# Kernel optimization log

Measured on AMD Instinct MI355X. Metric: run time of the kernel, lower is better.

Reference implementation:

```python
import jax, jax.numpy as jnp
import numpy as np

D_MODEL = 768
D_STATE = 16
D_CONV = 4
EXPAND = 2
D_INNER = EXPAND * D_MODEL          # 1536
DT_RANK = (D_MODEL + 15) // 16      # 48 (mamba default: ceil(d_model/16))


def setup_inputs() -> dict:
    key = jax.random.key(0)
    ks = jax.random.split(key, 8)
    B, T = 2, 1024
    s = 0.02
    return {
        "x": jax.random.normal(ks[0], (B, T, D_MODEL), jnp.float32),
        "ln_g": jnp.ones((D_MODEL,), jnp.float32),
        "ln_b": jnp.zeros((D_MODEL,), jnp.float32),
        "W_in": jax.random.normal(ks[1], (2 * D_INNER, D_MODEL), jnp.float32) * s,
        "conv_w": jax.random.normal(ks[2], (D_INNER, 1, D_CONV), jnp.float32) * s,
        "conv_b": jnp.zeros((D_INNER,), jnp.float32),
        "W_xproj": jax.random.normal(ks[3], (DT_RANK + 2 * D_STATE, D_INNER), jnp.float32) * s,
        "W_dt": jax.random.normal(ks[4], (D_INNER, DT_RANK), jnp.float32) * s,
        "b_dt": jax.random.normal(ks[5], (D_INNER,), jnp.float32) * s,
        "A_log": jnp.log(jnp.broadcast_to(jnp.arange(1.0, D_STATE + 1.0, dtype=jnp.float32), (D_INNER, D_STATE))),
        "Dp": jnp.ones((D_INNER,), jnp.float32),
        "W_out": jax.random.normal(ks[6], (D_MODEL, D_INNER), jnp.float32) * s,
    }


def _mamba_block(x, ln_g, ln_b, W_in, conv_w, conv_b, W_xproj, W_dt, b_dt, A_log, Dp, W_out):
    B, T, D = x.shape
    # LayerNorm
    mu = x.mean(-1, keepdims=True)
    var = ((x - mu) ** 2).mean(-1, keepdims=True)
    h = (x - mu) * jax.lax.rsqrt(var + 1e-5) * ln_g + ln_b
    # in_proj -> [B,T,2*d_inner], split into x-branch and gate z
    xz = h @ W_in.T
    xs, z = jnp.split(xz, 2, axis=-1)
    # causal depthwise conv over time (pad left d_conv-1), then SiLU
    xc = jax.lax.conv_general_dilated(
        xs.transpose(0, 2, 1), conv_w, (1,), [(D_CONV - 1, 0)],
        dimension_numbers=("NCH", "OIH", "NCH"), feature_group_count=D_INNER)
    xc = jax.nn.silu(xc.transpose(0, 2, 1) + conv_b)  # [B,T,d_inner]
    # x_proj -> dt_rank + 2*d_state
    x_dbl = xc @ W_xproj.T
    dt_r = x_dbl[..., :DT_RANK]
    Bm = x_dbl[..., DT_RANK:DT_RANK + D_STATE]       # [B,T,n]
    Cm = x_dbl[..., DT_RANK + D_STATE:]              # [B,T,n]
    dt = jax.nn.softplus(dt_r @ W_dt.T + b_dt)       # [B,T,d_inner]
    A = -jnp.exp(A_log)                              # [d_inner, n]
    dA = jnp.exp(jnp.einsum("btd,dn->btdn", dt, A))  # [B,T,d,n]
    dBu = jnp.einsum("btd,btn->btdn", dt * xc, Bm)   # [B,T,d,n]

    def step(s, inp):
        dA_t, dBu_t, C_t = inp
        s = dA_t * s + dBu_t                          # [B,d,n]
        y_t = jnp.einsum("bdn,bn->bd", s, C_t)
        return s, y_t

    s0 = jnp.zeros((B, D_INNER, D_STATE), x.dtype)
    _, ys = jax.lax.scan(step, s0,
                         (dA.transpose(1, 0, 2, 3), dBu.transpose(1, 0, 2, 3), Cm.transpose(1, 0, 2)))
    y = ys.transpose(1, 0, 2) + Dp * xc              # D skip connection
    y = y * jax.nn.silu(z)                           # gate
    return x + y @ W_out.T                           # out_proj + residual


def reference(x, ln_g, ln_b, W_in, conv_w, conv_b, W_xproj, W_dt, b_dt, A_log, Dp, W_out):
    return _mamba_block(x, ln_g, ln_b, W_in, conv_w, conv_b, W_xproj, W_dt, b_dt, A_log, Dp, W_out)
```

## Files before the change

kernel.cpp:

```cpp
#include <hip/hip_runtime.h>

typedef unsigned short u16;
typedef unsigned int u32;
typedef __attribute__((ext_vector_type(8))) short short8;
typedef __attribute__((ext_vector_type(4))) float f32x4;

#define D_MODEL 768
#define D_INNER 1536
#define D_XZ    3072
#define D_STATE 16
#define DT_RANK 48
#define NROW    2048
#define SEQ     1024
#define XDS     128
#define NCHUNK  128
#define CLEN    8

typedef const __attribute__((address_space(1))) u32 glb_u32;
typedef __attribute__((address_space(3))) u32 lds_u32;

__device__ __forceinline__ float bf2f(u16 u) {
    union { unsigned int i; float f; } v; v.i = ((unsigned int)u) << 16; return v.f;
}
__device__ __forceinline__ u16 f2bf(float f) {
    union { float f; unsigned int i; } v; v.f = f;
    unsigned int r = v.i + 0x7fffu + ((v.i >> 16) & 1u);
    return (u16)(r >> 16);
}
__device__ __forceinline__ void g2lds16(const u16* g, u16* l) {
    __builtin_amdgcn_global_load_lds((glb_u32*)g, (lds_u32*)l, 16, 0, 0);
}

#define N0 (D_XZ * D_MODEL / 4)
#define N1 (D_MODEL * D_INNER / 4)
#define N2 (XDS * D_INNER / 4)
#define N3 (D_INNER * 64 / 4)
#define N4 (D_INNER * D_STATE / 4)
#define N5 (NROW * XDS / 4)
#define N6 (NROW * D_MODEL / 4)
#define PREP_BLOCKS ((N0+N1+N2+N3+N4+N5+N6) / 256)
__global__ __launch_bounds__(256) void prep_ln_k(
    const float* __restrict__ x, const float* __restrict__ g,
    const float* __restrict__ bln, u16* __restrict__ h,
    const float* __restrict__ W_in, const float* __restrict__ W_out,
    const float* __restrict__ W_xp, const float* __restrict__ W_dt,
    const float* __restrict__ A_log,
    u16* __restrict__ Win_bf, u16* __restrict__ Wout_bf,
    u16* __restrict__ Wxp_bf, u16* __restrict__ Wdt_bf,
    float* __restrict__ negA, float* __restrict__ xdbl,
    float* __restrict__ outz)
{
    __shared__ float sred[4], sqred[4];
    int tid = threadIdx.x;
    if (blockIdx.x < NROW) {
        int row = blockIdx.x;
        const float* xr = x + (size_t)row * D_MODEL;
        float v[3], s = 0.f, sq = 0.f;
#pragma unroll
        for (int j = 0; j < 3; ++j) {
            v[j] = xr[tid + j * 256];
            s += v[j]; sq += v[j] * v[j];
        }
#pragma unroll
        for (int off = 32; off >= 1; off >>= 1) {
            s  += __shfl_xor(s,  off, 64);
            sq += __shfl_xor(sq, off, 64);
        }
        if ((tid & 63) == 0) { sred[tid >> 6] = s; sqred[tid >> 6] = sq; }
        __syncthreads();
        float st = sred[0] + sred[1] + sred[2] + sred[3];
        float sqt = sqred[0] + sqred[1] + sqred[2] + sqred[3];
        float mu = st * (1.f / D_MODEL);
        float var = sqt * (1.f / D_MODEL) - mu * mu;
        float rstd = rsqrtf(var + 1e-5f);
        u16* hr = h + (size_t)row * D_MODEL;
#pragma unroll
        for (int j = 0; j < 3; ++j) {
            int idx = tid + j * 256;
            hr[idx] = f2bf((v[j] - mu) * rstd * g[idx] + bln[idx]);
        }
        return;
    }
    int gid = (blockIdx.x - NROW) * 256 + tid;
    if (gid < N0) {
        float4 v = *(const float4*)(W_in + (size_t)gid * 4);
        u16* o = Win_bf + (size_t)gid * 4;
        o[0]=f2bf(v.x); o[1]=f2bf(v.y); o[2]=f2bf(v.z); o[3]=f2bf(v.w);
    } else if (gid < N0 + N1) {
        int i = gid - N0;
        float4 v = *(const float4*)(W_out + (size_t)i * 4);
        u16* o = Wout_bf + (size_t)i * 4;
        o[0]=f2bf(v.x); o[1]=f2bf(v.y); o[2]=f2bf(v.z); o[3]=f2bf(v.w);
    } else if (gid < N0 + N1 + N2) {
        int i = gid - N0 - N1;
        int n = (i * 4) / D_INNER, k = (i * 4) % D_INNER;
        u16* o = Wxp_bf + (size_t)i * 4;
        if (n < 80) {
            float4 v = *(const float4*)(W_xp + (size_t)n * D_INNER + k);
            o[0]=f2bf(v.x); o[1]=f2bf(v.y); o[2]=f2bf(v.z); o[3]=f2bf(v.w);
        } else { o[0]=0; o[1]=0; o[2]=0; o[3]=0; }
    } else if (gid < N0 + N1 + N2 + N3) {
        int i = gid - N0 - N1 - N2;
        int r = (i * 4) >> 6, c0 = (i * 4) & 63;
        u16* o = Wdt_bf + (size_t)i * 4;
        if (c0 < DT_RANK) {
            float4 v = *(const float4*)(W_dt + (size_t)r * DT_RANK + c0);
            o[0]=f2bf(v.x); o[1]=f2bf(v.y); o[2]=f2bf(v.z); o[3]=f2bf(v.w);
        } else { o[0]=0; o[1]=0; o[2]=0; o[3]=0; }
    } else if (gid < N0 + N1 + N2 + N3 + N4) {
        int i = gid - N0 - N1 - N2 - N3;
        float4 v = *(const float4*)(A_log + (size_t)i * 4);
        *(float4*)(negA + (size_t)i * 4) =
            make_float4(-__expf(v.x), -__expf(v.y), -__expf(v.z), -__expf(v.w));
    } else if (gid < N0 + N1 + N2 + N3 + N4 + N5) {
        int i = gid - N0 - N1 - N2 - N3 - N4;
        *(float4*)(xdbl + (size_t)i * 4) = make_float4(0.f, 0.f, 0.f, 0.f);
    } else {
        int i = gid - N0 - N1 - N2 - N3 - N4 - N5;
        *(float4*)(outz + (size_t)i * 4) = make_float4(0.f, 0.f, 0.f, 0.f);
    }
}

template<int MT, int NT, bool OUT_BF16>
__global__ __launch_bounds__(256) void gemm128(
    const u16* __restrict__ A, const u16* __restrict__ B,
    void* __restrict__ Cv, int M, int N, int K)
{
    constexpr int BM = 32 * MT, BN = 32 * NT;
    __shared__ __align__(16) u16 As[BM * 32];
    __shared__ __align__(16) u16 Bs[BN * 32];
    int tid = threadIdx.x, w = tid >> 6, lane = tid & 63;
    int wm = w & 1, wn = w >> 1;
    int m0 = blockIdx.x * BM, n0 = blockIdx.y * BN;
    int mloc = lane & 15, quad = lane >> 4;
    int lr = lane >> 2, lc = lane & 3;
    f32x4 acc[MT][NT] = {};

    for (int k0 = 0; k0 < K; k0 += 32) {
        __syncthreads();
#pragma unroll
        for (int j = w; j < 2 * MT; j += 4) {
            int row = j * 16 + lr;
            int cb = lc ^ ((row >> 1) & 3);
            g2lds16(A + (size_t)(m0 + row) * K + k0 + cb * 8, &As[j * 512]);
        }
#pragma unroll
        for (int j = w; j < 2 * NT; j += 4) {
            int row = j * 16 + lr;
            int cb = lc ^ ((row >> 1) & 3);
            g2lds16(B + (size_t)(n0 + row) * K + k0 + cb * 8, &Bs[j * 512]);
        }
        __syncthreads();
        short8 afr[MT], bfr[NT];
#pragma unroll
        for (int mt = 0; mt < MT; ++mt) {
            int row = wm * MT * 16 + mt * 16 + mloc;
            int cb = quad ^ ((row >> 1) & 3);
            afr[mt] = *(const short8*)(&As[row * 32 + cb * 8]);
        }
#pragma unroll
        for (int nt = 0; nt < NT; ++nt) {
            int row = wn * NT * 16 + nt * 16 + mloc;
            int cb = quad ^ ((row >> 1) & 3);
            bfr[nt] = *(const short8*)(&Bs[row * 32 + cb * 8]);
        }
#pragma unroll
        for (int mt = 0; mt < MT; ++mt)
#pragma unroll
            for (int nt = 0; nt < NT; ++nt)
                acc[mt][nt] = __builtin_amdgcn_mfma_f32_16x16x32_bf16(
                    afr[mt], bfr[nt], acc[mt][nt], 0, 0, 0);
    }
#pragma unroll
    for (int mt = 0; mt < MT; ++mt) {
        int grow0 = m0 + wm * MT * 16 + mt * 16 + quad * 4;
#pragma unroll
        for (int nt = 0; nt < NT; ++nt) {
            int gcol = n0 + wn * NT * 16 + nt * 16 + mloc;
#pragma unroll
            for (int r = 0; r < 4; ++r) {
                size_t idx = (size_t)(grow0 + r) * N + gcol;
                float v = acc[mt][nt][r];
                if (OUT_BF16) ((u16*)Cv)[idx] = f2bf(v);
                else          ((float*)Cv)[idx] = v;
            }
        }
    }
}

template<int MT, int NT, int KSLICE, bool ADD_X>
__global__ __launch_bounds__(256) void gemm_splitk(
    const u16* __restrict__ A, const u16* __restrict__ B,
    const float* __restrict__ X, float* __restrict__ Cout, int K, int CS)
{
    constexpr int BM = 32 * MT, BN = 32 * NT;
    __shared__ __align__(16) u16 As[BM * 32];
    __shared__ __align__(16) u16 Bs[BN * 32];
    int tid = threadIdx.x, w = tid >> 6, lane = tid & 63;
    int wm = w & 1, wn = w >> 1;
    int m0 = blockIdx.x * BM, n0 = blockIdx.y * BN;
    int kbase = blockIdx.z * KSLICE;
    int mloc = lane & 15, quad = lane >> 4;
    int lr = lane >> 2, lc = lane & 3;
    f32x4 acc[MT][NT] = {};

    for (int k0 = 0; k0 < KSLICE; k0 += 32) {
        __syncthreads();
#pragma unroll
        for (int j = w; j < 2 * MT; j += 4) {
            int row = j * 16 + lr;
            int cb = lc ^ ((row >> 1) & 3);
            g2lds16(A + (size_t)(m0 + row) * K + kbase + k0 + cb * 8, &As[j * 512]);
        }
#pragma unroll
        for (int j = w; j < 2 * NT; j += 4) {
            int row = j * 16 + lr;
            int cb = lc ^ ((row >> 1) & 3);
            g2lds16(B + (size_t)(n0 + row) * K + kbase + k0 + cb * 8, &Bs[j * 512]);
        }
        __syncthreads();
        short8 afr[MT], bfr[NT];
#pragma unroll
        for (int mt = 0; mt < MT; ++mt) {
            int row = wm * MT * 16 + mt * 16 + mloc;
            int cb = quad ^ ((row >> 1) & 3);
            afr[mt] = *(const short8*)(&As[row * 32 + cb * 8]);
        }
#pragma unroll
        for (int nt = 0; nt < NT; ++nt) {
            int row = wn * NT * 16 + nt * 16 + mloc;
            int cb = quad ^ ((row >> 1) & 3);
            bfr[nt] = *(const short8*)(&Bs[row * 32 + cb * 8]);
        }
#pragma unroll
        for (int mt = 0; mt < MT; ++mt)
#pragma unroll
            for (int nt = 0; nt < NT; ++nt)
                acc[mt][nt] = __builtin_amdgcn_mfma_f32_16x16x32_bf16(
                    afr[mt], bfr[nt], acc[mt][nt], 0, 0, 0);
    }
#pragma unroll
    for (int mt = 0; mt < MT; ++mt) {
        int grow0 = m0 + wm * MT * 16 + mt * 16 + quad * 4;
#pragma unroll
        for (int nt = 0; nt < NT; ++nt) {
            int gcol = n0 + wn * NT * 16 + nt * 16 + mloc;
#pragma unroll
            for (int r = 0; r < 4; ++r) {
                size_t idx = (size_t)(grow0 + r) * CS + gcol;
                float v = acc[mt][nt][r];
                if (ADD_X && blockIdx.z == 0) v += X[idx];
                unsafeAtomicAdd(&Cout[idx], v);
            }
        }
    }
}

__global__ __launch_bounds__(256) void dtgemm_k(
    const float* __restrict__ xdbl, const u16* __restrict__ Wdt,
    const float* __restrict__ bias, u16* __restrict__ dtout)
{
    __shared__ __align__(16) u16 Bs[64 * 72];
    int tid = threadIdx.x, wave = tid >> 6, lane = tid & 63;
    int m0 = blockIdx.x * 64, n0 = blockIdx.y * 64;
    int mloc = lane & 15, quad = lane >> 4;
    {
        int r = tid >> 3, ck = (tid & 7) * 8;
#pragma unroll
        for (int rr = 0; rr < 64; rr += 32) {
            int4 bv = *(const int4*)(Wdt + (size_t)(n0 + r + rr) * 64 + ck);
            *(int4*)(&Bs[(r + rr) * 72 + ck]) = bv;
        }
    }
    int arow = m0 + wave * 16 + mloc;
    const float* ar = xdbl + (size_t)arow * XDS + quad * 8;
    short8 af[2];
#pragma unroll
    for (int h = 0; h < 2; ++h) {
        float4 a0 = *(const float4*)(ar + h * 32);
        float4 a1 = *(const float4*)(ar + h * 32 + 4);
        short8 t;
        t[0]=(short)f2bf(a0.x); t[1]=(short)f2bf(a0.y);
        t[2]=(short)f2bf(a0.z); t[3]=(short)f2bf(a0.w);
        t[4]=(short)f2bf(a1.x); t[5]=(short)f2bf(a1.y);
        t[6]=(short)f2bf(a1.z); t[7]=(short)f2bf(a1.w);
        af[h] = t;
    }
    __syncthreads();
    f32x4 acc[4] = {};
#pragma unroll
    for (int h = 0; h < 2; ++h)
#pragma unroll
        for (int nt = 0; nt < 4; ++nt) {
            short8 bf = *(const short8*)(&Bs[(nt * 16 + mloc) * 72 + h * 32 + quad * 8]);
            acc[nt] = __builtin_amdgcn_mfma_f32_16x16x32_bf16(af[h], bf, acc[nt], 0, 0, 0);
        }
#pragma unroll
    for (int nt = 0; nt < 4; ++nt) {
        int gcol = n0 + nt * 16 + mloc;
        int grow = m0 + wave * 16 + quad * 4;
#pragma unroll
        for (int r = 0; r < 4; ++r) {
            float t = acc[nt][r] + bias[gcol];
            float sp = (t > 15.f) ? t : __logf(1.f + __expf(t));
            dtout[(size_t)(grow + r) * D_INNER + gcol] = f2bf(sp);
        }
    }
}

__global__ __launch_bounds__(256) void conv_silu_k(
    const u16* __restrict__ xz, const float* __restrict__ cw,
    const float* __restrict__ cb, u16* __restrict__ xc)
{
    int gid = blockIdx.x * 256 + threadIdx.x;
    int r = gid / (D_INNER / 4);
    int c4 = (gid - r * (D_INNER / 4)) * 4;
    int t = r & (SEQ - 1);
    float4 cbv = *(const float4*)(cb + c4);
    float acc[4] = {cbv.x, cbv.y, cbv.z, cbv.w};
    float4 wv[4];
#pragma unroll
    for (int j = 0; j < 4; ++j) wv[j] = *(const float4*)(cw + (c4 + j) * 4);
#pragma unroll
    for (int k = 0; k < 4; ++k) {
        int tt = t - 3 + k;
        if (tt >= 0) {
            ushort4 xv = *(const ushort4*)(xz + (size_t)(r - 3 + k) * D_XZ + c4);
            acc[0] += bf2f(xv.x) * ((const float*)&wv[0])[k];
            acc[1] += bf2f(xv.y) * ((const float*)&wv[1])[k];
            acc[2] += bf2f(xv.z) * ((const float*)&wv[2])[k];
            acc[3] += bf2f(xv.w) * ((const float*)&wv[3])[k];
        }
    }
    ushort4 o;
    o.x = f2bf(acc[0] / (1.f + __expf(-acc[0])));
    o.y = f2bf(acc[1] / (1.f + __expf(-acc[1])));
    o.z = f2bf(acc[2] / (1.f + __expf(-acc[2])));
    o.w = f2bf(acc[3] / (1.f + __expf(-acc[3])));
    *(ushort4*)(xc + (size_t)r * D_INNER + c4) = o;
}

__global__ __launch_bounds__(256) void scan_p1(
    const u16* __restrict__ dt, const u16* __restrict__ xc,
    const float* __restrict__ xdbl, const float* __restrict__ negA,
    float* __restrict__ Sbuf, float* __restrict__ dtsumbuf)
{
    __shared__ float Bsh[CLEN][D_STATE];
    int tid = threadIdx.x;
    int gid = blockIdx.x * 256 + tid;
    int d = gid % D_INNER;
    int bcN = gid / D_INNER;
    int c = bcN % NCHUNK, b = bcN / NCHUNK;
    size_t r0 = (size_t)b * SEQ + c * CLEN;
    if (tid < CLEN * D_STATE) {
        int tt = tid >> 4, n = tid & 15;
        Bsh[tt][n] = xdbl[(r0 + tt) * XDS + DT_RANK + n];
    }
    float a[D_STATE], s[D_STATE] = {};
    {
        const float4* Ar = (const float4*)(negA + d * D_STATE);
        float4 a0 = Ar[0], a1 = Ar[1], a2 = Ar[2], a3 = Ar[3];
        a[0]=a0.x; a[1]=a0.y; a[2]=a0.z; a[3]=a0.w;
        a[4]=a1.x; a[5]=a1.y; a[6]=a1.z; a[7]=a1.w;
        a[8]=a2.x; a[9]=a2.y; a[10]=a2.z; a[11]=a2.w;
        a[12]=a3.x; a[13]=a3.y; a[14]=a3.z; a[15]=a3.w;
    }
    float dtv[CLEN], du[CLEN];
    const u16* dp = dt + r0 * D_INNER + d;
    const u16* xp = xc + r0 * D_INNER + d;
#pragma unroll
    for (int t = 0; t < CLEN; ++t) {
        dtv[t] = bf2f(dp[t * D_INNER]);
        du[t] = dtv[t] * bf2f(xp[t * D_INNER]);
    }
    __syncthreads();
    float dtsum = 0.f;
#pragma unroll
    for (int t = 0; t < CLEN; ++t) {
        dtsum += dtv[t];
#pragma unroll
        for (int n = 0; n < D_STATE; ++n)
            s[n] = __expf(dtv[t] * a[n]) * s[n] + du[t] * Bsh[t][n];
    }
    float4* So = (float4*)(Sbuf + (size_t)gid * D_STATE);
#pragma unroll
    for (int j = 0; j < 4; ++j)
        So[j] = make_float4(s[j*4], s[j*4+1], s[j*4+2], s[j*4+3]);
    dtsumbuf[gid] = dtsum;
}

__global__ __launch_bounds__(256) void scan_p2(
    const float* __restrict__ Sbuf, const float* __restrict__ dtsumbuf,
    const float* __restrict__ negA, float* __restrict__ carry)
{
    int gid = blockIdx.x * 256 + threadIdx.x;
    int n = gid % D_STATE;
    int d = (gid / D_STATE) % D_INNER;
    int b = gid / (D_STATE * D_INNER);
    float a = negA[d * D_STATE + n];
    float s = 0.f;
#pragma unroll 8
    for (int c = 0; c < NCHUNK; ++c) {
        size_t idx = ((size_t)(b * NCHUNK + c) * D_INNER + d);
        carry[idx * D_STATE + n] = s;
        s = Sbuf[idx * D_STATE + n] + __expf(a * dtsumbuf[idx]) * s;
    }
}

__global__ __launch_bounds__(256) void scan_p3(
    const u16* __restrict__ dt, const u16* __restrict__ xc,
    const u16* __restrict__ xz, const float* __restrict__ xdbl,
    const float* __restrict__ negA, const float* __restrict__ Dp,
    const float* __restrict__ carry, u16* __restrict__ yy)
{
    __shared__ float BCsh[CLEN][2 * D_STATE];
    int tid = threadIdx.x;
    int gid = blockIdx.x * 256 + tid;
    int d = gid % D_INNER;
    int bcN = gid / D_INNER;
    int c = bcN % NCHUNK, b = bcN / NCHUNK;
    size_t r0 = (size_t)b * SEQ + c * CLEN;
    {
        int tt = tid >> 5, j = tid & 31;
        BCsh[tt][j] = xdbl[(r0 + tt) * XDS + DT_RANK + j];
    }
    float a[D_STATE], s[D_STATE];
    {
        const float4* Ci = (const float4*)(carry + (size_t)gid * D_STATE);
        float4 c0 = Ci[0], c1 = Ci[1], c2 = Ci[2], c3 = Ci[3];
        s[0]=c0.x; s[1]=c0.y; s[2]=c0.z; s[3]=c0.w;
        s[4]=c1.x; s[5]=c1.y; s[6]=c1.z; s[7]=c1.w;
        s[8]=c2.x; s[9]=c2.y; s[10]=c2.z; s[11]=c2.w;
        s[12]=c3.x; s[13]=c3.y; s[14]=c3.z; s[15]=c3.w;
        const float4* Ar = (const float4*)(negA + d * D_STATE);
        float4 a0 = Ar[0], a1 = Ar[1], a2 = Ar[2], a3 = Ar[3];
        a[0]=a0.x; a[1]=a0.y; a[2]=a0.z; a[3]=a0.w;
        a[4]=a1.x; a[5]=a1.y; a[6]=a1.z; a[7]=a1.w;
        a[8]=a2.x; a[9]=a2.y; a[10]=a2.z; a[11]=a2.w;
        a[12]=a3.x; a[13]=a3.y; a[14]=a3.z; a[15]=a3.w;
    }
    float dtv[CLEN], xcv[CLEN], zv[CLEN];
    const u16* dp = dt + r0 * D_INNER + d;
    const u16* xp = xc + r0 * D_INNER + d;
    const u16* zp = xz + r0 * D_XZ + D_INNER + d;
#pragma unroll
    for (int t = 0; t < CLEN; ++t) {
        dtv[t] = bf2f(dp[t * D_INNER]);
        xcv[t] = bf2f(xp[t * D_INNER]);
        zv[t]  = bf2f(zp[t * D_XZ]);
    }
    float dpv = Dp[d];
    __syncthreads();
    u16* yp = yy + r0 * D_INNER + d;
#pragma unroll
    for (int t = 0; t < CLEN; ++t) {
        float du = dtv[t] * xcv[t];
        float y = 0.f;
#pragma unroll
        for (int n = 0; n < D_STATE; ++n) {
            s[n] = __expf(dtv[t] * a[n]) * s[n] + du * BCsh[t][n];
            y += s[n] * BCsh[t][D_STATE + n];
        }
        float yv = y + dpv * xcv[t];
        float sig = 1.f / (1.f + __expf(-zv[t]));
        yp[t * D_INNER] = f2bf(yv * (zv[t] * sig));
    }
}

extern "C" void kernel_launch(void* const* d_in, const int* in_sizes, int n_in,
                              void* d_out, int out_size, void* d_ws, size_t ws_size,
                              hipStream_t stream) {
    const float* x      = (const float*)d_in[0];
    const float* ln_g   = (const float*)d_in[1];
    const float* ln_b   = (const float*)d_in[2];
    const float* W_in   = (const float*)d_in[3];
    const float* conv_w = (const float*)d_in[4];
    const float* conv_b = (const float*)d_in[5];
    const float* W_xp   = (const float*)d_in[6];
    const float* W_dt   = (const float*)d_in[7];
    const float* b_dt   = (const float*)d_in[8];
    const float* A_log  = (const float*)d_in[9];
    const float* Dp     = (const float*)d_in[10];
    const float* W_out  = (const float*)d_in[11];
    float* out = (float*)d_out;

    char* ws = (char*)d_ws;
    u16*   h_bf    = (u16*)ws;   ws += (size_t)NROW * D_MODEL * 2;
    u16*   xz_bf   = (u16*)ws;   ws += (size_t)NROW * D_XZ * 2;
    u16*   xc_bf   = (u16*)ws;   ws += (size_t)NROW * D_INNER * 2;
    float* xdbl    = (float*)ws; ws += (size_t)NROW * XDS * 4;
    u16*   dtbuf   = (u16*)ws;   ws += (size_t)NROW * D_INNER * 2;
    u16*   yybuf   = (u16*)ws;   ws += (size_t)NROW * D_INNER * 2;
    u16*   Win_bf  = (u16*)ws;   ws += (size_t)D_XZ * D_MODEL * 2;
    u16*   Wout_bf = (u16*)ws;   ws += (size_t)D_MODEL * D_INNER * 2;
    u16*   Wxp_bf  = (u16*)ws;   ws += (size_t)XDS * D_INNER * 2;
    u16*   Wdt_bf  = (u16*)ws;   ws += (size_t)D_INNER * 64 * 2;
    float* negA    = (float*)ws; ws += (size_t)D_INNER * D_STATE * 4;
    float* Sbuf    = (float*)ws; ws += (size_t)2 * NCHUNK * D_INNER * 16 * 4;
    float* dtsumb  = (float*)ws; ws += (size_t)2 * NCHUNK * D_INNER * 4;
    float* carryb  = (float*)ws;

    prep_ln_k<<<NROW + PREP_BLOCKS, 256, 0, stream>>>(
        x, ln_g, ln_b, h_bf, W_in, W_out, W_xp, W_dt, A_log,
        Win_bf, Wout_bf, Wxp_bf, Wdt_bf, negA, xdbl, out);

    gemm128<4, 2, true><<<dim3(NROW / 128, D_XZ / 64), 256, 0, stream>>>(
        h_bf, Win_bf, xz_bf, NROW, D_XZ, D_MODEL);
    conv_silu_k<<<NROW * (D_INNER / 4) / 256, 256, 0, stream>>>(
        xz_bf, conv_w, conv_b, xc_bf);
    gemm_splitk<2, 4, 192, false><<<dim3(NROW / 64, 1, 8), 256, 0, stream>>>(
        xc_bf, Wxp_bf, nullptr, xdbl, D_INNER, XDS);
    dtgemm_k<<<dim3(NROW / 64, D_INNER / 64), 256, 0, stream>>>(
        xdbl, Wdt_bf, b_dt, dtbuf);

    scan_p1<<<2 * NCHUNK * D_INNER / 256, 256, 0, stream>>>(
        dtbuf, xc_bf, xdbl, negA, Sbuf, dtsumb);
    scan_p2<<<2 * D_INNER * D_STATE / 256, 256, 0, stream>>>(
        Sbuf, dtsumb, negA, carryb);
    scan_p3<<<2 * NCHUNK * D_INNER / 256, 256, 0, stream>>>(
        dtbuf, xc_bf, xz_bf, xdbl, negA, Dp, carryb, yybuf);

    gemm_splitk<2, 2, 768, true><<<dim3(NROW / 64, D_MODEL / 64, 2), 256, 0, stream>>>(
        yybuf, Wout_bf, x, out, D_INNER, D_MODEL);
}
```

Baseline: 206.6 us.

## Fuse three-phase chunked scan into one cooperative kernel with grid syncs

Merges the chunk-local scan, the cross-chunk carry propagation and the output pass into a single cooperative kernel separated by grid-wide syncs. It keeps dt, xc, z and B/C in registers and LDS across phases instead of reloading them. Chunk length doubles and the chunk count halves so that 768 blocks can be co-resident, with launch bounds set to 3 blocks per CU. The costs are grid-sync overhead, higher register pressure from holding 16-step arrays, and a serial carry phase that only 192 of the 768 blocks execute.

```diff
diff --git a/kernel.cpp b/kernel.cpp
--- a/kernel.cpp
+++ b/kernel.cpp
@@ -1,4 +1,7 @@
 #include <hip/hip_runtime.h>
+#include <hip/hip_cooperative_groups.h>
+
+namespace cg = cooperative_groups;
 
 typedef unsigned short u16;
 typedef unsigned int u32;
@@ -13,8 +16,8 @@
 #define NROW    2048
 #define SEQ     1024
 #define XDS     128
-#define NCHUNK  128
-#define CLEN    8
+#define NCHUNK  64
+#define CLEN    16
 
 typedef const __attribute__((address_space(1))) u32 glb_u32;
 typedef __attribute__((address_space(3))) u32 lds_u32;
@@ -340,23 +343,28 @@
     *(ushort4*)(xc + (size_t)r * D_INNER + c4) = o;
 }
 
-__global__ __launch_bounds__(256) void scan_p1(
+__global__ __launch_bounds__(256, 3) void scan_fused(
     const u16* __restrict__ dt, const u16* __restrict__ xc,
-    const float* __restrict__ xdbl, const float* __restrict__ negA,
-    float* __restrict__ Sbuf, float* __restrict__ dtsumbuf)
+    const u16* __restrict__ xz, const float* __restrict__ xdbl,
+    const float* __restrict__ negA, const float* __restrict__ Dp,
+    float* __restrict__ Sbuf, float* __restrict__ dtsumbuf,
+    float* __restrict__ carry, u16* __restrict__ yy)
 {
-    __shared__ float Bsh[CLEN][D_STATE];
+    __shared__ float BCsh[CLEN][2 * D_STATE];
+    cg::grid_group grid = cg::this_grid();
     int tid = threadIdx.x;
     int gid = blockIdx.x * 256 + tid;
     int d = gid % D_INNER;
     int bcN = gid / D_INNER;
     int c = bcN % NCHUNK, b = bcN / NCHUNK;
     size_t r0 = (size_t)b * SEQ + c * CLEN;
-    if (tid < CLEN * D_STATE) {
-        int tt = tid >> 4, n = tid & 15;
-        Bsh[tt][n] = xdbl[(r0 + tt) * XDS + DT_RANK + n];
-    }
-    float a[D_STATE], s[D_STATE] = {};
+#pragma unroll
+    for (int j = 0; j < 2; ++j) {
+        int idx = tid + j * 256;
+        int row = idx >> 5, col = idx & 31;
+        BCsh[row][col] = xdbl[(r0 + row) * XDS + DT_RANK + col];
+    }
+    float a[D_STATE];
     {
         const float4* Ar = (const float4*)(negA + d * D_STATE);
         float4 a0 = Ar[0], a1 = Ar[1], a2 = Ar[2], a3 = Ar[3];
@@ -365,105 +373,75 @@
         a[8]=a2.x; a[9]=a2.y; a[10]=a2.z; a[11]=a2.w;
         a[12]=a3.x; a[13]=a3.y; a[14]=a3.z; a[15]=a3.w;
     }
-    float dtv[CLEN], du[CLEN];
-    const u16* dp = dt + r0 * D_INNER + d;
-    const u16* xp = xc + r0 * D_INNER + d;
-#pragma unroll
-    for (int t = 0; t < CLEN; ++t) {
-        dtv[t] = bf2f(dp[t * D_INNER]);
-        du[t] = dtv[t] * bf2f(xp[t * D_INNER]);
-    }
+    float dtv[CLEN], xcv[CLEN], zv[CLEN];
+    {
+        const u16* dp = dt + r0 * D_INNER + d;
+        const u16* xp = xc + r0 * D_INNER + d;
+        const u16* zp = xz + r0 * D_XZ + D_INNER + d;
+#pragma unroll
+        for (int t = 0; t < CLEN; ++t) {
+            dtv[t] = bf2f(dp[t * D_INNER]);
+            xcv[t] = bf2f(xp[t * D_INNER]);
+            zv[t]  = bf2f(zp[t * D_XZ]);
+        }
+    }
+    float dpv = Dp[d];
     __syncthreads();
-    float dtsum = 0.f;
-#pragma unroll
-    for (int t = 0; t < CLEN; ++t) {
-        dtsum += dtv[t];
-#pragma unroll
-        for (int n = 0; n < D_STATE; ++n)
-            s[n] = __expf(dtv[t] * a[n]) * s[n] + du[t] * Bsh[t][n];
-    }
-    float4* So = (float4*)(Sbuf + (size_t)gid * D_STATE);
-#pragma unroll
-    for (int j = 0; j < 4; ++j)
-        So[j] = make_float4(s[j*4], s[j*4+1], s[j*4+2], s[j*4+3]);
-    dtsumbuf[gid] = dtsum;
-}
-
-__global__ __launch_bounds__(256) void scan_p2(
-    const float* __restrict__ Sbuf, const float* __restrict__ dtsumbuf,
-    const float* __restrict__ negA, float* __restrict__ carry)
-{
-    int gid = blockIdx.x * 256 + threadIdx.x;
-    int n = gid % D_STATE;
-    int d = (gid / D_STATE) % D_INNER;
-    int b = gid / (D_STATE * D_INNER);
-    float a = negA[d * D_STATE + n];
-    float s = 0.f;
+    {
+        float s[D_STATE] = {};
+        float dtsum = 0.f;
+#pragma unroll
+        for (int t = 0; t < CLEN; ++t) {
+            dtsum += dtv[t];
+            float du = dtv[t] * xcv[t];
+#pragma unroll
+            for (int n = 0; n < D_STATE; ++n)
+                s[n] = __expf(dtv[t] * a[n]) * s[n] + du * BCsh[t][n];
+        }
+        float4* So = (float4*)(Sbuf + (size_t)gid * D_STATE);
+#pragma unroll
+        for (int j = 0; j < 4; ++j)
+            So[j] = make_float4(s[j*4], s[j*4+1], s[j*4+2], s[j*4+3]);
+        dtsumbuf[gid] = dtsum;
+    }
+    grid.sync();
+    if (blockIdx.x < (2 * D_INNER * D_STATE) / 256) {
+        int g2 = blockIdx.x * 256 + tid;
+        int n2 = g2 % D_STATE;
+        int d2 = (g2 / D_STATE) % D_INNER;
+        int b2 = g2 / (D_STATE * D_INNER);
+        float a2 = negA[d2 * D_STATE + n2];
+        float s = 0.f;
 #pragma unroll 8
-    for (int c = 0; c < NCHUNK; ++c) {
-        size_t idx = ((size_t)(b * NCHUNK + c) * D_INNER + d);
-        carry[idx * D_STATE + n] = s;
-        s = Sbuf[idx * D_STATE + n] + __expf(a * dtsumbuf[idx]) * s;
-    }
-}
-
-__global__ __launch_bounds__(256) void scan_p3(
-    const u16* __restrict__ dt, const u16* __restrict__ xc,
-    const u16* __restrict__ xz, const float* __restrict__ xdbl,
-    const float* __restrict__ negA, const float* __restrict__ Dp,
-    const float* __restrict__ carry, u16* __restrict__ yy)
-{
-    __shared__ float BCsh[CLEN][2 * D_STATE];
-    int tid = threadIdx.x;
-    int gid = blockIdx.x * 256 + tid;
-    int d = gid % D_INNER;
-    int bcN = gid / D_INNER;
-    int c = bcN % NCHUNK, b = bcN / NCHUNK;
-    size_t r0 = (size_t)b * SEQ + c * CLEN;
+        for (int cc = 0; cc < NCHUNK; ++cc) {
+            size_t idx = ((size_t)(b2 * NCHUNK + cc) * D_INNER + d2);
+            carry[idx * D_STATE + n2] = s;
+            s = Sbuf[idx * D_STATE + n2] + __expf(a2 * dtsumbuf[idx]) * s;
+        }
+    }
+    grid.sync();
     {
-        int tt = tid >> 5, j = tid & 31;
-        BCsh[tt][j] = xdbl[(r0 + tt) * XDS + DT_RANK + j];
-    }
-    float a[D_STATE], s[D_STATE];
-    {
+        float s[D_STATE];
         const float4* Ci = (const float4*)(carry + (size_t)gid * D_STATE);
         float4 c0 = Ci[0], c1 = Ci[1], c2 = Ci[2], c3 = Ci[3];
         s[0]=c0.x; s[1]=c0.y; s[2]=c0.z; s[3]=c0.w;
         s[4]=c1.x; s[5]=c1.y; s[6]=c1.z; s[7]=c1.w;
         s[8]=c2.x; s[9]=c2.y; s[10]=c2.z; s[11]=c2.w;
         s[12]=c3.x; s[13]=c3.y; s[14]=c3.z; s[15]=c3.w;
-        const float4* Ar = (const float4*)(negA + d * D_STATE);
-        float4 a0 = Ar[0], a1 = Ar[1], a2 = Ar[2], a3 = Ar[3];
-        a[0]=a0.x; a[1]=a0.y; a[2]=a0.z; a[3]=a0.w;
-        a[4]=a1.x; a[5]=a1.y; a[6]=a1.z; a[7]=a1.w;
-        a[8]=a2.x; a[9]=a2.y; a[10]=a2.z; a[11]=a2.w;
-        a[12]=a3.x; a[13]=a3.y; a[14]=a3.z; a[15]=a3.w;
-    }
-    float dtv[CLEN], xcv[CLEN], zv[CLEN];
-    const u16* dp = dt + r0 * D_INNER + d;
-    const u16* xp = xc + r0 * D_INNER + d;
-    const u16* zp = xz + r0 * D_XZ + D_INNER + d;
-#pragma unroll
-    for (int t = 0; t < CLEN; ++t) {
-        dtv[t] = bf2f(dp[t * D_INNER]);
-        xcv[t] = bf2f(xp[t * D_INNER]);
-        zv[t]  = bf2f(zp[t * D_XZ]);
-    }
-    float dpv = Dp[d];
-    __syncthreads();
-    u16* yp = yy + r0 * D_INNER + d;
-#pragma unroll
-    for (int t = 0; t < CLEN; ++t) {
-        float du = dtv[t] * xcv[t];
-        float y = 0.f;
-#pragma unroll
-        for (int n = 0; n < D_STATE; ++n) {
-            s[n] = __expf(dtv[t] * a[n]) * s[n] + du * BCsh[t][n];
-            y += s[n] * BCsh[t][D_STATE + n];
-        }
-        float yv = y + dpv * xcv[t];
-        float sig = 1.f / (1.f + __expf(-zv[t]));
-        yp[t * D_INNER] = f2bf(yv * (zv[t] * sig));
+        u16* yp = yy + r0 * D_INNER + d;
+#pragma unroll
+        for (int t = 0; t < CLEN; ++t) {
+            float du = dtv[t] * xcv[t];
+            float y = 0.f;
+#pragma unroll
+            for (int n = 0; n < D_STATE; ++n) {
+                s[n] = __expf(dtv[t] * a[n]) * s[n] + du * BCsh[t][n];
+                y += s[n] * BCsh[t][D_STATE + n];
+            }
+            float yv = y + dpv * xcv[t];
+            float sig = 1.f / (1.f + __expf(-zv[t]));
+            yp[t * D_INNER] = f2bf(yv * (zv[t] * sig));
+        }
     }
 }
 
@@ -513,12 +491,16 @@
     dtgemm_k<<<dim3(NROW / 64, D_INNER / 64), 256, 0, stream>>>(
         xdbl, Wdt_bf, b_dt, dtbuf);
 
-    scan_p1<<<2 * NCHUNK * D_INNER / 256, 256, 0, stream>>>(
-        dtbuf, xc_bf, xdbl, negA, Sbuf, dtsumb);
-    scan_p2<<<2 * D_INNER * D_STATE / 256, 256, 0, stream>>>(
-        Sbuf, dtsumb, negA, carryb);
-    scan_p3<<<2 * NCHUNK * D_INNER / 256, 256, 0, stream>>>(
-        dtbuf, xc_bf, xz_bf, xdbl, negA, Dp, carryb, yybuf);
+    {
+        void* args[] = {
+            (void*)&dtbuf, (void*)&xc_bf, (void*)&xz_bf, (void*)&xdbl,
+            (void*)&negA, (void*)&Dp, (void*)&Sbuf, (void*)&dtsumb,
+            (void*)&carryb, (void*)&yybuf
+        };
+        hipLaunchCooperativeKernel((void*)scan_fused,
+                                   dim3(2 * NCHUNK * D_INNER / 256), dim3(256),
+                                   args, 0, stream);
+    }
 
     gemm_splitk<2, 2, 768, true><<<dim3(NROW / 64, D_MODEL / 64, 2), 256, 0, stream>>>(
         yybuf, Wout_bf, x, out, D_INNER, D_MODEL);
```

Result: slower. 513.1 us (+148.3%).
